# Performance work log

Measured on AMD Instinct MI355X. Metric: run time of the kernel, lower is better.

The kernel has to match this reference:

```python
import jax, jax.numpy as jnp
import numpy as np

N, L, HID = 8192, 256, 128   # rows, input_len, hidden_size
H, NLIN = 2, 2               # n_heads, n_linear
EPS = 1e-5


def setup_inputs() -> dict:
    key = jax.random.key(0)
    ks = jax.random.split(key, 8)
    # attention params (torch.randn in source; scaled 0.02 for numerical sanity of softmax logits)
    Q = jax.random.normal(ks[0], (H, L, HID), jnp.float32) * 0.02
    K = jax.random.normal(ks[1], (H, L, HID), jnp.float32) * 0.02
    V_down = jax.random.normal(ks[2], (H, L, HID), jnp.float32) * 0.02
    V_up = jax.random.normal(ks[3], (H, HID, L), jnp.float32) * 0.02
    # nn.Linear(input_len, input_len): uniform(-1/sqrt(L), 1/sqrt(L))
    bnd = 1.0 / np.sqrt(L)
    W = jax.random.uniform(ks[4], (NLIN, L, L), jnp.float32, -bnd, bnd)
    b = jax.random.uniform(ks[5], (NLIN, L), jnp.float32, -bnd, bnd)
    x = jax.random.normal(ks[6], (N, L), jnp.float32)
    return {"x": x, "Q": Q, "K": K, "V_down": V_down, "V_up": V_up, "W": W, "b": b}


def _batch_norm(z):
    # custom BatchNorm1d: per-feature normalization over the batch (row) dim, no affine
    m = jnp.mean(z, axis=0, keepdims=True)
    v = jnp.var(z, axis=0, keepdims=True)
    return (z - m) * jax.lax.rsqrt(v + EPS)


def reference(x, Q, K, V_down, V_up, W, b):
    h = _batch_norm(x)                              # [N, L]
    dE = jnp.zeros_like(h)
    for i in range(Q.shape[0]):                     # small fixed head count
        q = h @ Q[i]                                # [N, HID]
        k = h @ K[i]                                # [N, HID]
        A = jax.nn.softmax(q @ k.T, axis=1)         # [N, N]
        dE = dE + A @ (h @ V_down[i]) @ V_up[i]     # low-rank value path
    h = _batch_norm(h + dE)
    for j in range(W.shape[0]):                     # per-row Linear+ReLU loop == batched matmul
        h = jax.nn.relu(h @ W[j].T + b[j])
    return h
```

## Files before the change

### kernel.cpp

```cpp
#include <hip/hip_runtime.h>
#include <hip/hip_bf16.h>

constexpr int Nrows = 8192;
constexpr int L     = 256;
constexpr int D     = 128;
constexpr float EPS = 1e-5f;

typedef __bf16 bf16x8 __attribute__((ext_vector_type(8)));
typedef __bf16 bf16x4 __attribute__((ext_vector_type(4)));
typedef float  f32x4  __attribute__((ext_vector_type(4)));

#define MFMA16(a, b, c) __builtin_amdgcn_mfma_f32_16x16x32_bf16((a), (b), (c), 0, 0, 0)

__global__ void k_cvt_params(const float* __restrict__ Q, const float* __restrict__ K,
                             const float* __restrict__ Vd, const float* __restrict__ Vup,
                             const float* __restrict__ W,
                             __bf16* __restrict__ Bt, __bf16* __restrict__ VupT,
                             __bf16* __restrict__ Wb) {
    int i = blockIdx.x * 256 + threadIdx.x;
    if (i < 6 * 128 * 256) {
        int g = i >> 15; int r = i & 32767; int d = r >> 8; int l = r & 255;
        const float* src = (g % 3 == 0 ? Q : (g % 3 == 1 ? K : Vd)) + (g / 3) * (L * D);
        Bt[i] = (__bf16)src[l * D + d];
    } else if (i < 8 * 128 * 256) {
        int j = i - 6 * 128 * 256;
        int h = j >> 15; int r = j & 32767; int l = r >> 7; int d = r & 127;
        VupT[j] = (__bf16)Vup[h * (D * L) + d * L + l];
    } else {
        int j = i - 8 * 128 * 256;
        Wb[j] = (__bf16)W[j];
    }
}

__global__ void k_bn_stats(const float* __restrict__ x, float* __restrict__ sum,
                           float* __restrict__ sq) {
    int col = threadIdx.x;
    int r0 = blockIdx.x * 64;
    float s = 0.f, s2 = 0.f;
    for (int i = 0; i < 64; i++) {
        float v = x[(r0 + i) * L + col];
        s += v; s2 += v * v;
    }
    atomicAdd(&sum[col], s);
    atomicAdd(&sq[col], s2);
}

__global__ void k_bn_norm1(const float* __restrict__ x, const float* __restrict__ sum,
                           const float* __restrict__ sq, __bf16* __restrict__ hb,
                           float* __restrict__ hf) {
    int i = (blockIdx.x * 256 + threadIdx.x) * 4;
    int col = i & (L - 1);
    f32x4 v = *(const f32x4*)(x + i);
    bf16x4 o; f32x4 of;
#pragma unroll
    for (int j = 0; j < 4; j++) {
        float m   = sum[col + j] * (1.0f / Nrows);
        float var = sq[col + j] * (1.0f / Nrows) - m * m;
        float rs  = rsqrtf(var + EPS);
        float t = (v[j] - m) * rs;
        of[j] = t; o[j] = (__bf16)t;
    }
    *(bf16x4*)(hb + i) = o;
    *(f32x4*)(hf + i) = of;
}

__global__ void k_bn_norm2(const float* __restrict__ z, const float* __restrict__ sum,
                           const float* __restrict__ sq, __bf16* __restrict__ h) {
    int i = (blockIdx.x * 256 + threadIdx.x) * 4;
    int col = i & (L - 1);
    f32x4 v = *(const f32x4*)(z + i);
    bf16x4 o;
#pragma unroll
    for (int j = 0; j < 4; j++) {
        float m   = sum[col + j] * (1.0f / Nrows);
        float var = sq[col + j] * (1.0f / Nrows) - m * m;
        float rs  = rsqrtf(var + EPS);
        o[j] = (__bf16)((v[j] - m) * rs);
    }
    *(bf16x4*)(h + i) = o;
}

__launch_bounds__(256)
__global__ void k_gemm_qkv(const __bf16* __restrict__ h, const __bf16* __restrict__ Bt,
                           __bf16* __restrict__ q0, __bf16* __restrict__ k0,
                           __bf16* __restrict__ q1, __bf16* __restrict__ k1,
                           __bf16* __restrict__ Vt) {
    int g = blockIdx.y;
    int m0 = blockIdx.x * 128;
    int w = threadIdx.x >> 6, lane = threadIdx.x & 63;
    int c = lane & 15, qd = lane >> 4;
    int mw = m0 + w * 32;
    const __bf16* B = Bt + g * (128 * 256);

    f32x4 acc[2][8] = {};
#pragma unroll
    for (int kc = 0; kc < 8; kc++) {
        bf16x8 a0 = *(const bf16x8*)(h + (mw + c) * L + kc * 32 + qd * 8);
        bf16x8 a1 = *(const bf16x8*)(h + (mw + 16 + c) * L + kc * 32 + qd * 8);
#pragma unroll
        for (int nt = 0; nt < 8; nt++) {
            bf16x8 b = *(const bf16x8*)(B + (nt * 16 + c) * L + kc * 32 + qd * 8);
            acc[0][nt] = MFMA16(a0, b, acc[0][nt]);
            acc[1][nt] = MFMA16(a1, b, acc[1][nt]);
        }
    }
    if (g == 2 || g == 5) {
        __bf16* vt = Vt + (g / 3) * (128 * Nrows);
#pragma unroll
        for (int mt = 0; mt < 2; mt++)
#pragma unroll
            for (int nt = 0; nt < 8; nt++)
#pragma unroll
                for (int r = 0; r < 4; r++) {
                    int row = mw + mt * 16 + 4 * qd + r;
                    int colv = nt * 16 + c;
                    vt[colv * Nrows + row] = (__bf16)acc[mt][nt][r];
                }
    } else {
        __bf16* dst = (g == 0) ? q0 : (g == 1) ? k0 : (g == 3) ? q1 : k1;
#pragma unroll
        for (int mt = 0; mt < 2; mt++)
#pragma unroll
            for (int nt = 0; nt < 8; nt++)
#pragma unroll
                for (int r = 0; r < 4; r++) {
                    int row = mw + mt * 16 + 4 * qd + r;
                    int colv = nt * 16 + c;
                    dst[row * D + colv] = (__bf16)acc[mt][nt][r];
                }
    }
}

__launch_bounds__(256, 1)
__global__ void k_flash(const __bf16* __restrict__ q0, const __bf16* __restrict__ k0,
                        const __bf16* __restrict__ q1, const __bf16* __restrict__ k1,
                        const __bf16* __restrict__ Vt, __bf16* __restrict__ O) {
    int head = blockIdx.x & 1;
    int qtile = blockIdx.x >> 1;
    int m0 = qtile * 64;
    const __bf16* qm = head ? q1 : q0;
    const __bf16* km = head ? k1 : k0;
    const __bf16* vt = Vt + head * (128 * Nrows);
    __bf16* Og = O + head * (Nrows * D);

    int w = threadIdx.x >> 6, lane = threadIdx.x & 63;
    int c = lane & 15, qd = lane >> 4;

    __shared__ __bf16 Pb[4][64 * 56];
    __shared__ float l_red[4][64];
    __shared__ float l_inv[64];
    __shared__ float obuf[4][64][16];

    bf16x8 aq[4][4];
#pragma unroll
    for (int mt = 0; mt < 4; mt++)
#pragma unroll
        for (int kc = 0; kc < 4; kc++)
            aq[mt][kc] = *(const bf16x8*)(qm + (m0 + mt * 16 + c) * D + kc * 32 + qd * 8);

    f32x4 oacc[4][8] = {};
    float lp[4][4] = {};
    __bf16* Pw = &Pb[w][0];

    for (int n0 = 0; n0 < Nrows; n0 += 128) {
        int nb = n0 + w * 32;
        bf16x8 kb[2][4], vb[8];
#pragma unroll
        for (int nt = 0; nt < 2; nt++)
#pragma unroll
            for (int kc = 0; kc < 4; kc++)
                kb[nt][kc] = *(const bf16x8*)(km + (nb + nt * 16 + c) * D + kc * 32 + qd * 8);
#pragma unroll
        for (int dvt = 0; dvt < 8; dvt++)
            vb[dvt] = *(const bf16x8*)(vt + (dvt * 16 + c) * Nrows + nb + qd * 8);

#pragma unroll
        for (int nt = 0; nt < 2; nt++) {
            f32x4 s[4] = {};
#pragma unroll
            for (int kc = 0; kc < 4; kc++) {
#pragma unroll
                for (int mt = 0; mt < 4; mt++) s[mt] = MFMA16(aq[mt][kc], kb[nt][kc], s[mt]);
            }
#pragma unroll
            for (int mt = 0; mt < 4; mt++)
#pragma unroll
                for (int r = 0; r < 4; r++) {
                    float e = __expf(s[mt][r]);
                    lp[mt][r] += e;
                    Pw[(mt * 16 + 4 * qd + r) * 56 + nt * 16 + c] = (__bf16)e;
                }
        }
        bf16x8 ap[4];
#pragma unroll
        for (int mt = 0; mt < 4; mt++)
            ap[mt] = *(const bf16x8*)(Pw + (mt * 16 + c) * 56 + qd * 8);
#pragma unroll
        for (int dvt = 0; dvt < 8; dvt++) {
#pragma unroll
            for (int mt = 0; mt < 4; mt++) oacc[mt][dvt] = MFMA16(ap[mt], vb[dvt], oacc[mt][dvt]);
        }
    }

#pragma unroll
    for (int mt = 0; mt < 4; mt++)
#pragma unroll
        for (int r = 0; r < 4; r++) {
            float v = lp[mt][r];
            v += __shfl_xor(v, 1, 16);
            v += __shfl_xor(v, 2, 16);
            v += __shfl_xor(v, 4, 16);
            v += __shfl_xor(v, 8, 16);
            lp[mt][r] = v;
        }
    if (c == 0) {
#pragma unroll
        for (int mt = 0; mt < 4; mt++)
#pragma unroll
            for (int r = 0; r < 4; r++)
                l_red[w][mt * 16 + 4 * qd + r] = lp[mt][r];
    }
    __syncthreads();
    if (threadIdx.x < 64)
        l_inv[threadIdx.x] = 1.0f / (l_red[0][threadIdx.x] + l_red[1][threadIdx.x] +
                                     l_red[2][threadIdx.x] + l_red[3][threadIdx.x]);

    for (int dvt = 0; dvt < 8; dvt++) {
        __syncthreads();
#pragma unroll
        for (int mt = 0; mt < 4; mt++)
#pragma unroll
            for (int r = 0; r < 4; r++)
                obuf[w][mt * 16 + 4 * qd + r][c] = oacc[mt][dvt][r];
        __syncthreads();
        int t = threadIdx.x;
        int row = (t * 4) >> 4, col = (t * 4) & 15;
        f32x4 v = *(const f32x4*)&obuf[0][row][col];
        f32x4 v1 = *(const f32x4*)&obuf[1][row][col];
        f32x4 v2 = *(const f32x4*)&obuf[2][row][col];
        f32x4 v3 = *(const f32x4*)&obuf[3][row][col];
        float il = l_inv[row];
        bf16x4 o;
#pragma unroll
        for (int e = 0; e < 4; e++) o[e] = (__bf16)((v[e] + v1[e] + v2[e] + v3[e]) * il);
        *(bf16x4*)(Og + (m0 + row) * D + dvt * 16 + col) = o;
    }
}

__launch_bounds__(256)
__global__ void k_gemm_vup(const __bf16* __restrict__ O, const __bf16* __restrict__ VupT,
                           const float* __restrict__ hf, float* __restrict__ z) {
    int n0 = blockIdx.y * 128;
    int m0 = blockIdx.x * 128;
    int w = threadIdx.x >> 6, lane = threadIdx.x & 63;
    int c = lane & 15, qd = lane >> 4;
    int mw = m0 + w * 32;

    f32x4 acc[2][8] = {};
#pragma unroll
    for (int kc = 0; kc < 8; kc++) {
        const __bf16* Oh = O + (kc >> 2) * (Nrows * D);
        const __bf16* Vh = VupT + (kc >> 2) * (L * D);
        int ko = (kc & 3) * 32 + qd * 8;
        bf16x8 a0 = *(const bf16x8*)(Oh + (mw + c) * D + ko);
        bf16x8 a1 = *(const bf16x8*)(Oh + (mw + 16 + c) * D + ko);
#pragma unroll
        for (int nt = 0; nt < 8; nt++) {
            bf16x8 b = *(const bf16x8*)(Vh + (n0 + nt * 16 + c) * D + ko);
            acc[0][nt] = MFMA16(a0, b, acc[0][nt]);
            acc[1][nt] = MFMA16(a1, b, acc[1][nt]);
        }
    }
#pragma unroll
    for (int mt = 0; mt < 2; mt++)
#pragma unroll
        for (int nt = 0; nt < 8; nt++)
#pragma unroll
            for (int r = 0; r < 4; r++) {
                int row = mw + mt * 16 + 4 * qd + r;
                int col = n0 + nt * 16 + c;
                z[row * L + col] = acc[mt][nt][r] + hf[row * L + col];
            }
}

template <typename OutT>
__launch_bounds__(256)
__global__ void k_gemm_w(const __bf16* __restrict__ hin, const __bf16* __restrict__ W,
                         const float* __restrict__ bias, OutT* __restrict__ out) {
    int n0 = blockIdx.y * 128;
    int m0 = blockIdx.x * 128;
    int w = threadIdx.x >> 6, lane = threadIdx.x & 63;
    int c = lane & 15, qd = lane >> 4;
    int mw = m0 + w * 32;

    f32x4 acc[2][8] = {};
#pragma unroll
    for (int kc = 0; kc < 8; kc++) {
        bf16x8 a0 = *(const bf16x8*)(hin + (mw + c) * L + kc * 32 + qd * 8);
        bf16x8 a1 = *(const bf16x8*)(hin + (mw + 16 + c) * L + kc * 32 + qd * 8);
#pragma unroll
        for (int nt = 0; nt < 8; nt++) {
            bf16x8 b = *(const bf16x8*)(W + (n0 + nt * 16 + c) * L + kc * 32 + qd * 8);
            acc[0][nt] = MFMA16(a0, b, acc[0][nt]);
            acc[1][nt] = MFMA16(a1, b, acc[1][nt]);
        }
    }
#pragma unroll
    for (int mt = 0; mt < 2; mt++)
#pragma unroll
        for (int nt = 0; nt < 8; nt++) {
            int col = n0 + nt * 16 + c;
            float bv = bias[col];
#pragma unroll
            for (int r = 0; r < 4; r++) {
                int row = mw + mt * 16 + 4 * qd + r;
                float v = fmaxf(acc[mt][nt][r] + bv, 0.0f);
                out[row * L + col] = (OutT)v;
            }
        }
}

extern "C" void kernel_launch(void* const* d_in, const int* in_sizes, int n_in,
                              void* d_out, int out_size, void* d_ws, size_t ws_size,
                              hipStream_t stream) {
    (void)in_sizes; (void)n_in; (void)out_size; (void)ws_size;
    const float* x   = (const float*)d_in[0];
    const float* Q   = (const float*)d_in[1];
    const float* K   = (const float*)d_in[2];
    const float* Vd  = (const float*)d_in[3];
    const float* Vup = (const float*)d_in[4];
    const float* W   = (const float*)d_in[5];
    const float* b   = (const float*)d_in[6];
    float* out = (float*)d_out;

    char* ws = (char*)d_ws;
    size_t off = 0;
    auto alloc = [&](size_t bytes) -> void* {
        void* p = ws + off;
        off += (bytes + 255) & ~(size_t)255;
        return p;
    };
    float*  stats = (float*)alloc(4 * 256 * sizeof(float));
    __bf16* Bt    = (__bf16*)alloc(6 * 128 * 256 * 2);
    __bf16* VupT  = (__bf16*)alloc(2 * 256 * 128 * 2);
    __bf16* Wb    = (__bf16*)alloc(2 * 256 * 256 * 2);
    __bf16* hb    = (__bf16*)alloc((size_t)Nrows * L * 2);
    float*  hf    = (float*)alloc((size_t)Nrows * L * 4);
    __bf16* q0    = (__bf16*)alloc((size_t)Nrows * D * 2);
    __bf16* k0    = (__bf16*)alloc((size_t)Nrows * D * 2);
    __bf16* q1    = (__bf16*)alloc((size_t)Nrows * D * 2);
    __bf16* k1    = (__bf16*)alloc((size_t)Nrows * D * 2);
    __bf16* Vt    = (__bf16*)alloc((size_t)2 * 128 * Nrows * 2);
    __bf16* O     = (__bf16*)alloc((size_t)2 * Nrows * D * 2);
    float*  z     = (float*)alloc((size_t)Nrows * L * 4);
    __bf16* h2    = (__bf16*)alloc((size_t)Nrows * L * 2);
    __bf16* h3    = (__bf16*)alloc((size_t)Nrows * L * 2);

    float* sum1 = stats, *sq1 = stats + 256, *sum2 = stats + 512, *sq2 = stats + 768;

    hipMemsetAsync(stats, 0, 4 * 256 * sizeof(float), stream);
    k_cvt_params<<<1536, 256, 0, stream>>>(Q, K, Vd, Vup, W, Bt, VupT, Wb);
    k_bn_stats<<<128, 256, 0, stream>>>(x, sum1, sq1);
    k_bn_norm1<<<2048, 256, 0, stream>>>(x, sum1, sq1, hb, hf);
    k_gemm_qkv<<<dim3(64, 6), 256, 0, stream>>>(hb, Bt, q0, k0, q1, k1, Vt);
    k_flash<<<256, 256, 0, stream>>>(q0, k0, q1, k1, Vt, O);
    k_gemm_vup<<<dim3(64, 2), 256, 0, stream>>>(O, VupT, hf, z);
    k_bn_stats<<<128, 256, 0, stream>>>(z, sum2, sq2);
    k_bn_norm2<<<2048, 256, 0, stream>>>(z, sum2, sq2, h2);
    k_gemm_w<__bf16><<<dim3(64, 2), 256, 0, stream>>>(h2, Wb, b, h3);
    k_gemm_w<float><<<dim3(64, 2), 256, 0, stream>>>(h3, Wb + 256 * 256, b + 256, out);
}
```

Baseline: 327.4 us.

## Split flash attention over key range and combine partial sums in a new kernel

```diff
diff --git a/kernel.cpp b/kernel.cpp
--- a/kernel.cpp
+++ b/kernel.cpp
@@ -5,6 +5,7 @@
 constexpr int L     = 256;
 constexpr int D     = 128;
 constexpr float EPS = 1e-5f;
+constexpr int KSPLIT = 2;
 
 typedef __bf16 bf16x8 __attribute__((ext_vector_type(8)));
 typedef __bf16 bf16x4 __attribute__((ext_vector_type(4)));
@@ -131,24 +132,26 @@
     }
 }
 
-__launch_bounds__(256, 1)
+__launch_bounds__(256, 2)
 __global__ void k_flash(const __bf16* __restrict__ q0, const __bf16* __restrict__ k0,
                         const __bf16* __restrict__ q1, const __bf16* __restrict__ k1,
-                        const __bf16* __restrict__ Vt, __bf16* __restrict__ O) {
+                        const __bf16* __restrict__ Vt, float* __restrict__ Opart,
+                        float* __restrict__ Lpart) {
     int head = blockIdx.x & 1;
-    int qtile = blockIdx.x >> 1;
+    int qtile = (blockIdx.x >> 1) & 127;
+    int split = blockIdx.x >> 8;
     int m0 = qtile * 64;
     const __bf16* qm = head ? q1 : q0;
     const __bf16* km = head ? k1 : k0;
     const __bf16* vt = Vt + head * (128 * Nrows);
-    __bf16* Og = O + head * (Nrows * D);
+    float* Op = Opart + (size_t)split * (2 * Nrows * D) + (size_t)head * (Nrows * D);
+    float* Lp = Lpart + split * (2 * Nrows) + head * Nrows;
 
     int w = threadIdx.x >> 6, lane = threadIdx.x & 63;
     int c = lane & 15, qd = lane >> 4;
 
     __shared__ __bf16 Pb[4][64 * 56];
     __shared__ float l_red[4][64];
-    __shared__ float l_inv[64];
     __shared__ float obuf[4][64][16];
 
     bf16x8 aq[4][4];
@@ -162,7 +165,9 @@
     float lp[4][4] = {};
     __bf16* Pw = &Pb[w][0];
 
-    for (int n0 = 0; n0 < Nrows; n0 += 128) {
+    int n_begin = split * (Nrows / KSPLIT);
+    int n_end = n_begin + Nrows / KSPLIT;
+    for (int n0 = n_begin; n0 < n_end; n0 += 128) {
         int nb = n0 + w * 32;
         bf16x8 kb[2][4], vb[8];
 #pragma unroll
@@ -177,11 +182,13 @@
 #pragma unroll
         for (int nt = 0; nt < 2; nt++) {
             f32x4 s[4] = {};
+            __builtin_amdgcn_s_setprio(1);
 #pragma unroll
             for (int kc = 0; kc < 4; kc++) {
 #pragma unroll
                 for (int mt = 0; mt < 4; mt++) s[mt] = MFMA16(aq[mt][kc], kb[nt][kc], s[mt]);
             }
+            __builtin_amdgcn_s_setprio(0);
 #pragma unroll
             for (int mt = 0; mt < 4; mt++)
 #pragma unroll
@@ -195,11 +202,13 @@
 #pragma unroll
         for (int mt = 0; mt < 4; mt++)
             ap[mt] = *(const bf16x8*)(Pw + (mt * 16 + c) * 56 + qd * 8);
+        __builtin_amdgcn_s_setprio(1);
 #pragma unroll
         for (int dvt = 0; dvt < 8; dvt++) {
 #pragma unroll
             for (int mt = 0; mt < 4; mt++) oacc[mt][dvt] = MFMA16(ap[mt], vb[dvt], oacc[mt][dvt]);
         }
+        __builtin_amdgcn_s_setprio(0);
     }
 
 #pragma unroll
@@ -221,9 +230,10 @@
                 l_red[w][mt * 16 + 4 * qd + r] = lp[mt][r];
     }
     __syncthreads();
-    if (threadIdx.x < 64)
-        l_inv[threadIdx.x] = 1.0f / (l_red[0][threadIdx.x] + l_red[1][threadIdx.x] +
-                                     l_red[2][threadIdx.x] + l_red[3][threadIdx.x]);
+    if (threadIdx.x < 64) {
+        int t = threadIdx.x;
+        Lp[m0 + t] = l_red[0][t] + l_red[1][t] + l_red[2][t] + l_red[3][t];
+    }
 
     for (int dvt = 0; dvt < 8; dvt++) {
         __syncthreads();
@@ -239,12 +249,25 @@
         f32x4 v1 = *(const f32x4*)&obuf[1][row][col];
         f32x4 v2 = *(const f32x4*)&obuf[2][row][col];
         f32x4 v3 = *(const f32x4*)&obuf[3][row][col];
-        float il = l_inv[row];
-        bf16x4 o;
-#pragma unroll
-        for (int e = 0; e < 4; e++) o[e] = (__bf16)((v[e] + v1[e] + v2[e] + v3[e]) * il);
-        *(bf16x4*)(Og + (m0 + row) * D + dvt * 16 + col) = o;
-    }
+        f32x4 o;
+#pragma unroll
+        for (int e = 0; e < 4; e++) o[e] = v[e] + v1[e] + v2[e] + v3[e];
+        *(f32x4*)(Op + (size_t)(m0 + row) * D + dvt * 16 + col) = o;
+    }
+}
+
+__global__ void k_att_combine(const float* __restrict__ Opart, const float* __restrict__ Lpart,
+                              __bf16* __restrict__ O) {
+    int i = blockIdx.x * 256 + threadIdx.x;
+    int base = i * 4;
+    int gr = base >> 7;
+    f32x4 a = *(const f32x4*)(Opart + base);
+    f32x4 c = *(const f32x4*)(Opart + (size_t)2 * Nrows * D + base);
+    float linv = 1.0f / (Lpart[gr] + Lpart[2 * Nrows + gr]);
+    bf16x4 o;
+#pragma unroll
+    for (int e = 0; e < 4; e++) o[e] = (__bf16)((a[e] + c[e]) * linv);
+    *(bf16x4*)(O + base) = o;
 }
 
 __launch_bounds__(256)
@@ -352,6 +375,8 @@
     __bf16* k1    = (__bf16*)alloc((size_t)Nrows * D * 2);
     __bf16* Vt    = (__bf16*)alloc((size_t)2 * 128 * Nrows * 2);
     __bf16* O     = (__bf16*)alloc((size_t)2 * Nrows * D * 2);
+    float*  Opart = (float*)alloc((size_t)KSPLIT * 2 * Nrows * D * 4);
+    float*  Lpart = (float*)alloc((size_t)KSPLIT * 2 * Nrows * 4);
     float*  z     = (float*)alloc((size_t)Nrows * L * 4);
     __bf16* h2    = (__bf16*)alloc((size_t)Nrows * L * 2);
     __bf16* h3    = (__bf16*)alloc((size_t)Nrows * L * 2);
@@ -363,7 +388,8 @@
     k_bn_stats<<<128, 256, 0, stream>>>(x, sum1, sq1);
     k_bn_norm1<<<2048, 256, 0, stream>>>(x, sum1, sq1, hb, hf);
     k_gemm_qkv<<<dim3(64, 6), 256, 0, stream>>>(hb, Bt, q0, k0, q1, k1, Vt);
-    k_flash<<<256, 256, 0, stream>>>(q0, k0, q1, k1, Vt, O);
+    k_flash<<<256 * KSPLIT, 256, 0, stream>>>(q0, k0, q1, k1, Vt, Opart, Lpart);
+    k_att_combine<<<2048, 256, 0, stream>>>(Opart, Lpart, O);
     k_gemm_vup<<<dim3(64, 2), 256, 0, stream>>>(O, VupT, hf, z);
     k_bn_stats<<<128, 256, 0, stream>>>(z, sum2, sq2);
     k_bn_norm2<<<2048, 256, 0, stream>>>(z, sum2, sq2, h2);
```

Result: slower. 497.2 us (+51.8%).
